# Kernel optimization log

Hardware: AMD Instinct MI355X
Metric: run time of the kernel (lower is better)

The kernel has to match this reference:

```python
import jax, jax.numpy as jnp
import numpy as np

E = 32          # n_routed_experts / num_local_experts
H = 1024        # hidden_size
I = 512         # moe_intermediate_size
G = 8           # n_group
TKG = 4         # topk_group
TOPK = 8        # num_experts_per_tok
NSH = 2         # n_shared_experts
SCALE = 2.5     # routed_scaling_factor


def setup_inputs() -> dict:
    key = jax.random.key(0)
    ks = jax.random.split(key, 10)
    s = 0.02
    return {
        "hidden_states": jax.random.normal(ks[0], (2, 1024, H), jnp.float32),
        # router: linear weight [E, H] and e_score_correction_bias [E]
        "gate_w": jax.random.normal(ks[1], (E, H), jnp.float32) * s,
        "gate_bias": jax.random.normal(ks[2], (E,), jnp.float32) * s,
        # routed experts (stacked SwiGLU weights, torch Linear layout [out, in])
        "w_gate": jax.random.normal(ks[3], (E, I, H), jnp.float32) * s,
        "w_up": jax.random.normal(ks[4], (E, I, H), jnp.float32) * s,
        "w_down": jax.random.normal(ks[5], (E, H, I), jnp.float32) * s,
        # shared experts: one MLP with intermediate = I * NSH
        "sh_gate": jax.random.normal(ks[6], (I * NSH, H), jnp.float32) * s,
        "sh_up": jax.random.normal(ks[7], (I * NSH, H), jnp.float32) * s,
        "sh_down": jax.random.normal(ks[8], (H, I * NSH), jnp.float32) * s,
    }


def reference(hidden_states, gate_w, gate_bias, w_gate, w_up, w_down,
              sh_gate, sh_up, sh_down):
    B, S, Hd = hidden_states.shape
    h = hidden_states.reshape(-1, Hd)                      # [T, H]

    # ---- router (DeepseekV3TopkRouter + route_tokens_to_experts) ----
    logits = h.astype(jnp.float32) @ gate_w.T              # [T, E]
    scores = jax.nn.sigmoid(logits)
    sc = scores + gate_bias                                # scores_for_choice
    # group score = sum of top-2 expert scores within each group
    grp = sc.reshape(-1, G, E // G)                        # [T, G, E/G]
    group_scores = jax.lax.top_k(grp, 2)[0].sum(-1)        # [T, G]
    gidx = jax.lax.top_k(group_scores, TKG)[1]             # [T, TKG]
    gmask = jnp.sum(jax.nn.one_hot(gidx, G, dtype=sc.dtype), axis=1)  # [T, G]
    smask = jnp.repeat(gmask, E // G, axis=1)              # [T, E]
    masked = jnp.where(smask > 0, sc, jnp.zeros_like(sc))  # masked_fill(~mask, 0)
    tki = jax.lax.top_k(masked, TOPK)[1]                   # [T, TOPK]
    tkw = jnp.take_along_axis(scores, tki, axis=1)         # gather raw sigmoid scores
    tkw = tkw / (tkw.sum(-1, keepdims=True) + 1e-20)       # norm_topk_prob
    tkw = tkw * SCALE

    # ---- dispatch-compute-combine (experts_forward) ----
    # combine[t, e] = sum_k tkw[t, k] * [tki[t, k] == e]
    combine = (jax.nn.one_hot(tki, E, dtype=tkw.dtype) * tkw[..., None]).sum(1)  # [T, E]
    g = jax.nn.silu(jnp.einsum('th,eih->tei', h, w_gate))  # [T, E, I]
    u = jnp.einsum('th,eih->tei', h, w_up)                 # [T, E, I]
    routed = jnp.einsum('tei,ehi->th', g * u * combine[:, :, None], w_down)  # [T, H]

    # ---- shared experts ----
    sg = jax.nn.silu(h @ sh_gate.T)
    shared = (sg * (h @ sh_up.T)) @ sh_down.T              # [T, H]

    return (routed + shared).reshape(B, S, Hd)
```

## Files before the change

kernel.cpp:

```cpp
#include <hip/hip_runtime.h>
#include <hip/hip_bf16.h>
#include <cstdint>

#define E_ 32
#define H_ 1024
#define I_ 512
#define G_ 8
#define NSH_ 2
#define SCALE_ 2.5f
#define NROUTED (E_ * I_)
#define PADCAP (16384 + E_ * 128)

typedef unsigned short u16;
using bf16x8_t = __attribute__((ext_vector_type(8))) __bf16;
using f32x4_t  = __attribute__((ext_vector_type(4))) float;

__device__ __forceinline__ u16 f2bf(float x) {
  union { float f; uint32_t u; } v; v.f = x;
  uint32_t u = v.u;
  uint32_t r = (u + 0x7fffu + ((u >> 16) & 1u)) >> 16;
  return (u16)r;
}
__device__ __forceinline__ float bf2f(u16 x) {
  union { uint32_t u; float f; } v; v.u = ((uint32_t)x) << 16; return v.f;
}

__device__ __forceinline__ void load_lds16(const void* g, void* l) {
  __builtin_amdgcn_global_load_lds(
      (const __attribute__((address_space(1))) unsigned int*)g,
      (__attribute__((address_space(3))) unsigned int*)l,
      16, 0, 0);
}

#define OFF_BU   16777216L
#define OFF_BD   33554432L
#define OFF_BSHG 50331648L
#define OFF_BSHU 51380224L
#define OFF_BSHD 52428800L
#define WBF_TOT  53477376L

#define W4_WG  4194304L
#define W4_WU  8388608L
#define W4_WD  12582912L
#define W4_SHG 12845056L
#define W4_SHU 13107200L
#define W4_TOT 13369344L
__global__ void prep_kernel(const float* __restrict__ gw, float* __restrict__ gwT,
                            int* __restrict__ counts, int* __restrict__ cursor,
                            int* __restrict__ qheads,
                            int* __restrict__ tok_list, float* __restrict__ wt_list,
                            const float* __restrict__ wg, const float* __restrict__ wu,
                            const float* __restrict__ wd, const float* __restrict__ shg,
                            const float* __restrict__ shu, const float* __restrict__ shd,
                            u16* __restrict__ wbf) {
  long i0 = (long)blockIdx.x * blockDim.x + threadIdx.x;
  if (i0 < H_ * E_) {
    int k = (int)(i0 >> 5), e = (int)(i0 & 31);
    gwT[i0] = gw[(long)e * H_ + k];
  }
  if (i0 < PADCAP) { tok_list[i0] = 0; wt_list[i0] = 0.f; }
  if (i0 < E_) { counts[i0] = 0; cursor[i0] = 0; }
  if (i0 < 2) qheads[i0] = 0;

  long stride = (long)gridDim.x * blockDim.x;
  for (long i = i0; i < W4_TOT; i += stride) {
    const float* s; long off; long dofs;
    if (i < W4_WG)       { s = wg;  off = i;            dofs = off * 4; }
    else if (i < W4_WU)  { s = wu;  off = i - W4_WG;    dofs = OFF_BU + off * 4; }
    else if (i < W4_WD)  { s = wd;  off = i - W4_WU;    dofs = OFF_BD + off * 4; }
    else if (i < W4_SHG) { s = shg; off = i - W4_WD;    dofs = OFF_BSHG + off * 4; }
    else if (i < W4_SHU) { s = shu; off = i - W4_SHG;   dofs = OFF_BSHU + off * 4; }
    else                 { s = shd; off = i - W4_SHU;   dofs = OFF_BSHD + off * 4; }
    float4 v = ((const float4*)s)[off];
    ushort4 o;
    o.x = f2bf(v.x); o.y = f2bf(v.y); o.z = f2bf(v.z); o.w = f2bf(v.w);
    *(ushort4*)(wbf + dofs) = o;
  }
}

__global__ __launch_bounds__(256) void logits_kernel(
    const float* __restrict__ h, const float* __restrict__ gwT,
    float* __restrict__ lpart,
    u16* __restrict__ hbf, int T) {
  __shared__ float shh[64][128];
  __shared__ float shw[128][E_];
  const int tid = threadIdx.x;
  const int t0 = blockIdx.x * 64;
  const int k0 = blockIdx.y * 128;
  #pragma unroll
  for (int i = 0; i < 8; ++i) {
    int c = tid + 256 * i;
    int row = c >> 5, col = c & 31;
    float4 v = *(const float4*)(h + (size_t)(t0 + row) * H_ + k0 + col * 4);
    *(float4*)(&shh[row][col * 4]) = v;
    ushort4 o;
    o.x = f2bf(v.x); o.y = f2bf(v.y); o.z = f2bf(v.z); o.w = f2bf(v.w);
    *(ushort4*)(hbf + (size_t)(t0 + row) * H_ + k0 + col * 4) = o;
  }
  #pragma unroll
  for (int i = 0; i < 4; ++i) {
    int c = tid + 256 * i;
    int row = c >> 3, col = c & 7;
    *(float4*)(&shw[row][col * 4]) =
        *(const float4*)(gwT + (size_t)(k0 + row) * E_ + col * 4);
  }
  __syncthreads();
  const int e = tid & 31;
  const int tb = (tid >> 5) * 8;
  float acc[8] = {0.f, 0.f, 0.f, 0.f, 0.f, 0.f, 0.f, 0.f};
  #pragma unroll 4
  for (int k = 0; k < 128; ++k) {
    float wv = shw[k][e];
    #pragma unroll
    for (int j = 0; j < 8; ++j) acc[j] += shh[tb + j][k] * wv;
  }
  #pragma unroll
  for (int j = 0; j < 8; ++j)
    lpart[((size_t)blockIdx.y * T + (t0 + tb + j)) * E_ + e] = acc[j];
}

__global__ __launch_bounds__(256) void topk_kernel(
    const float* __restrict__ lpart, const float* __restrict__ gb,
    int* __restrict__ idx8, float* __restrict__ wt8, int* __restrict__ counts,
    int T) {
  const int tid = threadIdx.x;
  const int l = tid & 63, wid = tid >> 6;
  const int e = l & 31, half = l >> 5;
  const int t = blockIdx.x * 8 + wid * 2 + half;

  float lg = 0.f;
  #pragma unroll
  for (int s = 0; s < 8; ++s) lg += lpart[((size_t)s * T + t) * E_ + e];
  float score = 1.f / (1.f + __expf(-lg));
  float sc = score + gb[e];

  float x1 = __shfl_xor(sc, 1);
  float x2 = __shfl_xor(sc, 2);
  float x3 = __shfl_xor(sc, 3);
  float hi1 = fmaxf(sc, x1), lo1 = fminf(sc, x1);
  float hi2 = fmaxf(x2, x3), lo2 = fminf(x2, x3);
  float m1 = fmaxf(hi1, hi2);
  float m2 = (hi1 >= hi2) ? fmaxf(lo1, hi2) : fmaxf(lo2, hi1);
  float gs = m1 + m2;

  float ga[8];
  #pragma unroll
  for (int g = 0; g < 8; ++g) ga[g] = __shfl(gs, (half << 5) + g * 4);
  unsigned gm = 0;
  #pragma unroll
  for (int r = 0; r < 4; ++r) {
    float bv = -1e30f; int bi = 0;
    #pragma unroll
    for (int g = 0; g < 8; ++g)
      if (!((gm >> g) & 1u) && ga[g] > bv) { bv = ga[g]; bi = g; }
    gm |= 1u << bi;
  }
  float msk = ((gm >> (e >> 2)) & 1u) ? sc : 0.f;

  float wsum = 0.f, myw = 0.f;
  int myi = 0;
  #pragma unroll
  for (int r = 0; r < 8; ++r) {
    float av = msk; int ai = e;
    #pragma unroll
    for (int m = 16; m; m >>= 1) {
      float ov = __shfl_xor(av, m);
      int oi = __shfl_xor(ai, m);
      if (ov > av || (ov == av && oi < ai)) { av = ov; ai = oi; }
    }
    float wscore = __shfl(score, (half << 5) + ai);
    wsum += wscore;
    if (e == r) { myi = ai; myw = wscore; }
    if (e == ai) msk = 0.f;
  }
  float inv = SCALE_ / (wsum + 1e-20f);
  if (e < 8) {
    idx8[(size_t)t * 8 + e] = myi;
    wt8[(size_t)t * 8 + e] = myw * inv;
    atomicAdd(&counts[myi], 1);
  }
}

__global__ void fill_kernel(const int* __restrict__ idx8, const float* __restrict__ wt8,
                            const int* __restrict__ counts, int* __restrict__ cursor,
                            int* __restrict__ tok_list, float* __restrict__ wt_list,
                            int* __restrict__ pair_pos, int npair) {
  int i = blockIdx.x * blockDim.x + threadIdx.x;
  if (i >= npair) return;
  int e = idx8[i];
  int offz = 0;
  for (int k = 0; k < E_; ++k) {
    if (k == e) break;
    offz += ((counts[k] + 127) >> 7) << 7;
  }
  int p = atomicAdd(&cursor[e], 1);
  int slot = offz + p;
  tok_list[slot] = i >> 3;
  wt_list[slot] = wt8[i];
  pair_pos[i] = slot;
}

__global__ __launch_bounds__(256, 2) void p1_kernel(
    const u16* __restrict__ hbf,
    const u16* __restrict__ wbf,
    const int* __restrict__ counts,
    const int* __restrict__ tok_list, const float* __restrict__ wt_list,
    int* __restrict__ qheads,
    u16* __restrict__ gu,
    u16* __restrict__ gu_sh,
    int T) {
  __shared__ u16 lsA[2][128 * 32];
  __shared__ u16 lsB0[2][128 * 32];
  __shared__ u16 lsB1[2][128 * 32];
  __shared__ int s_tok[128];
  __shared__ float s_wt[128];
  __shared__ int s_off[E_], s_ntt[E_];
  __shared__ int s_tot, s_tile;

  const int tid = threadIdx.x;
  if (tid == 0) {
    int run = 0, tot = 0;
    for (int e = 0; e < E_; ++e) {
      s_off[e] = run;
      int nt = (counts[e] + 127) >> 7;
      s_ntt[e] = nt;
      run += nt << 7;
      tot += nt * 4;
    }
    s_tot = tot + (T / 128) * 8;
  }

  const int w = tid >> 6, l = tid & 63;
  const int wr = w >> 1, wc = w & 1;
  const int lr = l & 15, lh = l >> 4;
  const int rdblk = (lh ^ ((lr >> 1) & 3)) << 3;

  const int c0 = tid, c1 = tid + 256;
  const int row0 = c0 >> 2, cb0 = c0 & 3, scb0 = cb0 ^ ((row0 >> 1) & 3);
  const int row1 = c1 >> 2, cb1 = c1 & 3, scb1 = cb1 ^ ((row1 >> 1) & 3);

  for (;;) {
    __syncthreads();
    if (tid == 0) s_tile = atomicAdd(&qheads[0], 1);
    __syncthreads();
    int q = s_tile;
    if (q >= s_tot) break;

    int z = 0, rem = q;
    for (; z < E_; ++z) { int t = s_ntt[z] * 4; if (rem < t) break; rem -= t; }
    const bool sh_e = (z == E_);
    int tt, nb;
    if (sh_e) { tt = rem >> 3; nb = rem & 7; }
    else      { tt = rem >> 2; nb = rem & 3; }
    const int off = sh_e ? 0 : s_off[z];

    if (tid < 128) {
      if (sh_e) { s_tok[tid] = tt * 128 + tid; s_wt[tid] = 1.0f; }
      else {
        int slot = off + tt * 128 + tid;
        s_tok[tid] = tok_list[slot];
        s_wt[tid] = wt_list[slot];
      }
    }
    __syncthreads();

    const u16* Bg = sh_e ? (wbf + OFF_BSHG + (size_t)(nb * 128) * H_)
                         : (wbf + ((size_t)z * I_ + nb * 128) * H_);
    const u16* Bu = sh_e ? (wbf + OFF_BSHU + (size_t)(nb * 128) * H_)
                         : (wbf + OFF_BU + ((size_t)z * I_ + nb * 128) * H_);
    const u16* A0 = hbf + (size_t)s_tok[row0] * H_ + scb0 * 8;
    const u16* A1 = hbf + (size_t)s_tok[row1] * H_ + scb1 * 8;

    f32x4_t acc0[4][4], acc1[4][4];
    #pragma unroll
    for (int m = 0; m < 4; ++m)
      #pragma unroll
      for (int n = 0; n < 4; ++n) {
        acc0[m][n] = (f32x4_t){0.f, 0.f, 0.f, 0.f};
        acc1[m][n] = (f32x4_t){0.f, 0.f, 0.f, 0.f};
      }

    auto stage = [&](int b, int k0) {
      load_lds16(A0 + k0, (char*)&lsA[b][0] + c0 * 16);
      load_lds16(A1 + k0, (char*)&lsA[b][0] + c1 * 16);
      load_lds16(Bg + (size_t)row0 * H_ + k0 + scb0 * 8, (char*)&lsB0[b][0] + c0 * 16);
      load_lds16(Bg + (size_t)row1 * H_ + k0 + scb1 * 8, (char*)&lsB0[b][0] + c1 * 16);
      load_lds16(Bu + (size_t)row0 * H_ + k0 + scb0 * 8, (char*)&lsB1[b][0] + c0 * 16);
      load_lds16(Bu + (size_t)row1 * H_ + k0 + scb1 * 8, (char*)&lsB1[b][0] + c1 * 16);
    };
    auto compute = [&](int b) {
      bf16x8_t af[4], b0f[4], b1f[4];
      #pragma unroll
      for (int m = 0; m < 4; ++m)
        af[m] = *(const bf16x8_t*)(&lsA[b][0] + (wr * 64 + m * 16 + lr) * 32 + rdblk);
      #pragma unroll
      for (int n = 0; n < 4; ++n) {
        b0f[n] = *(const bf16x8_t*)(&lsB0[b][0] + (wc * 64 + n * 16 + lr) * 32 + rdblk);
        b1f[n] = *(const bf16x8_t*)(&lsB1[b][0] + (wc * 64 + n * 16 + lr) * 32 + rdblk);
      }
      #pragma unroll
      for (int m = 0; m < 4; ++m)
        #pragma unroll
        for (int n = 0; n < 4; ++n) {
          acc0[m][n] = __builtin_amdgcn_mfma_f32_16x16x32_bf16(af[m], b0f[n], acc0[m][n], 0, 0, 0);
          acc1[m][n] = __builtin_amdgcn_mfma_f32_16x16x32_bf16(af[m], b1f[n], acc1[m][n], 0, 0, 0);
        }
    };

    stage(0, 0);
    __syncthreads();
    int cur = 0;
    #pragma unroll 1
    for (int s = 0; s < 32; ++s) {
      if (s < 31) stage(cur ^ 1, (s + 1) * 32);
      compute(cur);
      __syncthreads();
      cur ^= 1;
    }

    const int ldo = sh_e ? (I_ * NSH_) : I_;
    u16* outp = sh_e ? (gu_sh + (size_t)(tt * 128) * ldo + nb * 128)
                     : (gu + (size_t)(off + tt * 128) * ldo + nb * 128);
    #pragma unroll
    for (int m = 0; m < 4; ++m) {
      #pragma unroll
      for (int n = 0; n < 4; ++n) {
        int col = wc * 64 + n * 16 + lr;
        #pragma unroll
        for (int j = 0; j < 4; ++j) {
          int trow = wr * 64 + m * 16 + lh * 4 + j;
          float gv = acc0[m][n][j], uv = acc1[m][n][j];
          float sv = gv / (1.f + __expf(-gv));
          outp[(size_t)trow * ldo + col] = f2bf(sv * uv * s_wt[trow]);
        }
      }
    }
  }
}

__global__ __launch_bounds__(256, 3) void p2_kernel(
    const u16* __restrict__ gu, const u16* __restrict__ gu_sh,
    const u16* __restrict__ wbf,
    const int* __restrict__ counts,
    int* __restrict__ qheads,
    u16* __restrict__ part,
    u16* __restrict__ part_sh,
    int T) {
  __shared__ u16 lsA[2][128 * 32];
  __shared__ u16 lsB[2][128 * 32];
  __shared__ int s_off[E_], s_ntt[E_];
  __shared__ int s_tot, s_tile;

  const int tid = threadIdx.x;
  if (tid == 0) {
    int run = 0, tot = 0;
    for (int e = 0; e < E_; ++e) {
      s_off[e] = run;
      int nt = (counts[e] + 127) >> 7;
      s_ntt[e] = nt;
      run += nt << 7;
      tot += nt * 8;
    }
    s_tot = tot + (T / 128) * 8;
  }

  const int w = tid >> 6, l = tid & 63;
  const int wr = w >> 1, wc = w & 1;
  const int lr = l & 15, lh = l >> 4;
  const int rdblk = (lh ^ ((lr >> 1) & 3)) << 3;

  const int c0 = tid, c1 = tid + 256;
  const int row0 = c0 >> 2, cb0 = c0 & 3, scb0 = cb0 ^ ((row0 >> 1) & 3);
  const int row1 = c1 >> 2, cb1 = c1 & 3, scb1 = cb1 ^ ((row1 >> 1) & 3);

  for (;;) {
    __syncthreads();
    if (tid == 0) s_tile = atomicAdd(&qheads[1], 1);
    __syncthreads();
    int q = s_tile;
    if (q >= s_tot) break;

    int z = 0, rem = q;
    for (; z < E_; ++z) { int t = s_ntt[z] * 8; if (rem < t) break; rem -= t; }
    const bool sh_e = (z == E_);
    int tt = rem >> 3, nb = rem & 7;

    const int K = sh_e ? (I_ * NSH_) : I_;
    const int NT = K / 32;
    const u16* Ab = sh_e ? (gu_sh + (size_t)(tt * 128) * K)
                         : (gu + (size_t)(s_off[z] + tt * 128) * K);
    const u16* Bb = sh_e ? (wbf + OFF_BSHD + (size_t)(nb * 128) * K)
                         : (wbf + OFF_BD + (size_t)z * H_ * I_ + (size_t)(nb * 128) * K);
    u16* outp = sh_e ? (part_sh + (size_t)(tt * 128) * H_ + nb * 128)
                     : (part + (size_t)(s_off[z] + tt * 128) * H_ + nb * 128);

    f32x4_t acc[4][4];
    #pragma unroll
    for (int m = 0; m < 4; ++m)
      #pragma unroll
      for (int n = 0; n < 4; ++n) acc[m][n] = (f32x4_t){0.f, 0.f, 0.f, 0.f};

    auto stage = [&](int b, int k0) {
      load_lds16(Ab + (size_t)row0 * K + k0 + scb0 * 8, (char*)&lsA[b][0] + c0 * 16);
      load_lds16(Ab + (size_t)row1 * K + k0 + scb1 * 8, (char*)&lsA[b][0] + c1 * 16);
      load_lds16(Bb + (size_t)row0 * K + k0 + scb0 * 8, (char*)&lsB[b][0] + c0 * 16);
      load_lds16(Bb + (size_t)row1 * K + k0 + scb1 * 8, (char*)&lsB[b][0] + c1 * 16);
    };
    auto compute = [&](int b) {
      bf16x8_t af[4], bf[4];
      #pragma unroll
      for (int m = 0; m < 4; ++m)
        af[m] = *(const bf16x8_t*)(&lsA[b][0] + (wr * 64 + m * 16 + lr) * 32 + rdblk);
      #pragma unroll
      for (int n = 0; n < 4; ++n)
        bf[n] = *(const bf16x8_t*)(&lsB[b][0] + (wc * 64 + n * 16 + lr) * 32 + rdblk);
      #pragma unroll
      for (int m = 0; m < 4; ++m)
        #pragma unroll
        for (int n = 0; n < 4; ++n)
          acc[m][n] = __builtin_amdgcn_mfma_f32_16x16x32_bf16(af[m], bf[n], acc[m][n], 0, 0, 0);
    };

    stage(0, 0);
    __syncthreads();
    int cur = 0;
    #pragma unroll 1
    for (int s = 0; s < NT; ++s) {
      if (s < NT - 1) stage(cur ^ 1, (s + 1) * 32);
      compute(cur);
      __syncthreads();
      cur ^= 1;
    }

    #pragma unroll
    for (int m = 0; m < 4; ++m) {
      #pragma unroll
      for (int n = 0; n < 4; ++n) {
        int col = wc * 64 + n * 16 + lr;
        #pragma unroll
        for (int j = 0; j < 4; ++j) {
          int trow = wr * 64 + m * 16 + lh * 4 + j;
          outp[(size_t)trow * H_ + col] = f2bf(acc[m][n][j]);
        }
      }
    }
  }
}

__global__ void combine_kernel(const u16* __restrict__ part, const u16* __restrict__ part_sh,
                               const int* __restrict__ pair_pos, float* __restrict__ out) {
  int t = blockIdx.x;
  int h = threadIdx.x * 4;
  int pp[8];
  #pragma unroll
  for (int s = 0; s < 8; ++s) pp[s] = pair_pos[(long)t * 8 + s];
  ushort4 v = *(const ushort4*)(part_sh + (size_t)t * H_ + h);
  float a0 = bf2f(v.x), a1 = bf2f(v.y), a2 = bf2f(v.z), a3 = bf2f(v.w);
  #pragma unroll
  for (int s = 0; s < 8; ++s) {
    ushort4 u = *(const ushort4*)(part + (size_t)pp[s] * H_ + h);
    a0 += bf2f(u.x); a1 += bf2f(u.y); a2 += bf2f(u.z); a3 += bf2f(u.w);
  }
  float4 o = {a0, a1, a2, a3};
  *(float4*)(out + (size_t)t * H_ + h) = o;
}

extern "C" void kernel_launch(void* const* d_in, const int* in_sizes, int n_in,
                              void* d_out, int out_size, void* d_ws, size_t ws_size,
                              hipStream_t stream) {
  const float* hs  = (const float*)d_in[0];
  const float* gw  = (const float*)d_in[1];
  const float* gb  = (const float*)d_in[2];
  const float* wg  = (const float*)d_in[3];
  const float* wu  = (const float*)d_in[4];
  const float* wd  = (const float*)d_in[5];
  const float* shg = (const float*)d_in[6];
  const float* shu = (const float*)d_in[7];
  const float* shd = (const float*)d_in[8];
  float* out = (float*)d_out;

  const int T = in_sizes[0] / H_;

  char* ws = (char*)d_ws;
  size_t off = 0;
  auto alloc = [&](size_t bytes) {
    char* p = ws + off;
    off += (bytes + 255) & ~(size_t)255;
    return p;
  };
  int*   counts   = (int*)alloc(E_ * 4);
  int*   cursor   = (int*)alloc(E_ * 4);
  int*   qheads   = (int*)alloc(2 * 4);
  int*   idx8     = (int*)alloc((size_t)T * 8 * 4);
  float* wt8      = (float*)alloc((size_t)T * 8 * 4);
  int*   pair_pos = (int*)alloc((size_t)T * 8 * 4);
  int*   tok_list = (int*)alloc(PADCAP * 4);
  float* wt_list  = (float*)alloc(PADCAP * 4);
  float* gwT      = (float*)alloc((size_t)H_ * E_ * 4);
  float* lpart    = (float*)alloc((size_t)8 * T * E_ * 4);
  u16* hbf     = (u16*)alloc((size_t)T * H_ * 2);
  u16* wbf     = (u16*)alloc((size_t)WBF_TOT * 2);
  u16* gu      = (u16*)alloc((size_t)PADCAP * I_ * 2);
  u16* gu_sh   = (u16*)alloc((size_t)T * I_ * NSH_ * 2);
  u16* part    = (u16*)alloc((size_t)PADCAP * H_ * 2);
  u16* part_sh = (u16*)alloc((size_t)T * H_ * 2);
  if (off > ws_size) return;

  hipLaunchKernelGGL(prep_kernel, dim3(4096), dim3(256), 0, stream,
                     gw, gwT, counts, cursor, qheads, tok_list, wt_list,
                     wg, wu, wd, shg, shu, shd, wbf);

  hipLaunchKernelGGL(logits_kernel, dim3(T / 64, 8), dim3(256), 0, stream,
                     hs, gwT, lpart, hbf, T);

  hipLaunchKernelGGL(topk_kernel, dim3(T / 8), dim3(256), 0, stream,
                     lpart, gb, idx8, wt8, counts, T);

  hipLaunchKernelGGL(fill_kernel, dim3((T * 8 + 255) / 256), dim3(256), 0, stream,
                     idx8, wt8, counts, cursor, tok_list, wt_list, pair_pos, T * 8);

  hipLaunchKernelGGL(p1_kernel, dim3(512), dim3(256), 0, stream,
                     hbf, wbf, counts, tok_list, wt_list, qheads, gu, gu_sh, T);

  hipLaunchKernelGGL(p2_kernel, dim3(768), dim3(256), 0, stream,
                     gu, gu_sh, wbf, counts, qheads, part, part_sh, T);

  hipLaunchKernelGGL(combine_kernel, dim3(T), dim3(256), 0, stream,
                     part, part_sh, pair_pos, out);
}
```

Baseline: 268.5 us.

## Triple-buffer LDS staging in both expert GEMM kernels with one barrier per step

Both grouped GEMM kernels move from double to triple LDS buffering. The fetch runs two K-steps ahead, and explicit vmcnt waits plus a single s_barrier per iteration replace the old trailing __syncthreads. The goal is to hide more global-load latency and remove one full sync per K-step. The cost is more LDS per block, which could cut occupancy, and the hand-counted vmcnt values must match the number of loads issued per stage.

```diff
diff --git a/kernel.cpp b/kernel.cpp
--- a/kernel.cpp
+++ b/kernel.cpp
@@ -209,9 +209,9 @@
     u16* __restrict__ gu,
     u16* __restrict__ gu_sh,
     int T) {
-  __shared__ u16 lsA[2][128 * 32];
-  __shared__ u16 lsB0[2][128 * 32];
-  __shared__ u16 lsB1[2][128 * 32];
+  __shared__ u16 lsA[3][128 * 32];
+  __shared__ u16 lsB0[3][128 * 32];
+  __shared__ u16 lsB1[3][128 * 32];
   __shared__ int s_tok[128];
   __shared__ float s_wt[128];
   __shared__ int s_off[E_], s_ntt[E_];
@@ -280,7 +280,8 @@
         acc1[m][n] = (f32x4_t){0.f, 0.f, 0.f, 0.f};
       }
 
-    auto stage = [&](int b, int k0) {
+    auto stage = [&](int b, int ks) {
+      int k0 = ks * 32;
       load_lds16(A0 + k0, (char*)&lsA[b][0] + c0 * 16);
       load_lds16(A1 + k0, (char*)&lsA[b][0] + c1 * 16);
       load_lds16(Bg + (size_t)row0 * H_ + k0 + scb0 * 8, (char*)&lsB0[b][0] + c0 * 16);
@@ -308,15 +309,19 @@
     };
 
     stage(0, 0);
-    __syncthreads();
-    int cur = 0;
+    stage(1, 1);
+    int b0 = 0, b1 = 1, b2 = 2;
     #pragma unroll 1
-    for (int s = 0; s < 32; ++s) {
-      if (s < 31) stage(cur ^ 1, (s + 1) * 32);
-      compute(cur);
-      __syncthreads();
-      cur ^= 1;
-    }
+    for (int s = 0; s < 31; ++s) {
+      asm volatile("s_waitcnt vmcnt(6)" ::: "memory");
+      __builtin_amdgcn_s_barrier();
+      compute(b0);
+      if (s < 30) stage(b2, s + 2);
+      int tb = b0; b0 = b1; b1 = b2; b2 = tb;
+    }
+    asm volatile("s_waitcnt vmcnt(0)" ::: "memory");
+    __builtin_amdgcn_s_barrier();
+    compute(b0);
 
     const int ldo = sh_e ? (I_ * NSH_) : I_;
     u16* outp = sh_e ? (gu_sh + (size_t)(tt * 128) * ldo + nb * 128)
@@ -346,8 +351,8 @@
     u16* __restrict__ part,
     u16* __restrict__ part_sh,
     int T) {
-  __shared__ u16 lsA[2][128 * 32];
-  __shared__ u16 lsB[2][128 * 32];
+  __shared__ u16 lsA[3][128 * 32];
+  __shared__ u16 lsB[3][128 * 32];
   __shared__ int s_off[E_], s_ntt[E_];
   __shared__ int s_tot, s_tile;
 
@@ -400,7 +405,8 @@
       #pragma unroll
       for (int n = 0; n < 4; ++n) acc[m][n] = (f32x4_t){0.f, 0.f, 0.f, 0.f};
 
-    auto stage = [&](int b, int k0) {
+    auto stage = [&](int b, int ks) {
+      int k0 = ks * 32;
       load_lds16(Ab + (size_t)row0 * K + k0 + scb0 * 8, (char*)&lsA[b][0] + c0 * 16);
       load_lds16(Ab + (size_t)row1 * K + k0 + scb1 * 8, (char*)&lsA[b][0] + c1 * 16);
       load_lds16(Bb + (size_t)row0 * K + k0 + scb0 * 8, (char*)&lsB[b][0] + c0 * 16);
@@ -422,15 +428,19 @@
     };
 
     stage(0, 0);
-    __syncthreads();
-    int cur = 0;
+    stage(1, 1);
+    int b0 = 0, b1 = 1, b2 = 2;
     #pragma unroll 1
-    for (int s = 0; s < NT; ++s) {
-      if (s < NT - 1) stage(cur ^ 1, (s + 1) * 32);
-      compute(cur);
-      __syncthreads();
-      cur ^= 1;
-    }
+    for (int s = 0; s < NT - 1; ++s) {
+      asm volatile("s_waitcnt vmcnt(4)" ::: "memory");
+      __builtin_amdgcn_s_barrier();
+      compute(b0);
+      if (s + 2 < NT) stage(b2, s + 2);
+      int tb = b0; b0 = b1; b1 = b2; b2 = tb;
+    }
+    asm volatile("s_waitcnt vmcnt(0)" ::: "memory");
+    __builtin_amdgcn_s_barrier();
+    compute(b0);
 
     #pragma unroll
     for (int m = 0; m < 4; ++m) {
```

Measured after the change: 266.4 us. About the same (-0.8%).

## Retile expert GEMMs to BK=64 single-buffered with N-major tile order

Applied to the files above, without the earlier changes.

Both grouped GEMM kernels move from a double-buffered K=32 pipeline to a single-buffered K=64 stage with an 8-way XOR swizzle. p1 narrows its N tile from 128 to 64 so it fits three blocks per CU. Tile indices are reordered so consecutive tiles share the same weight slice across token tiles, which should improve L2 reuse of expert weights. Persistent grid sizes grow to match the higher occupancy. Dropping the double buffer loses the overlap of loads with compute inside a block, and the design relies on the extra resident blocks to hide that latency instead.

```diff
diff --git a/kernel.cpp b/kernel.cpp
--- a/kernel.cpp
+++ b/kernel.cpp
@@ -200,7 +200,7 @@
   pair_pos[i] = slot;
 }
 
-__global__ __launch_bounds__(256, 2) void p1_kernel(
+__global__ __launch_bounds__(256, 3) void p1_kernel(
     const u16* __restrict__ hbf,
     const u16* __restrict__ wbf,
     const int* __restrict__ counts,
@@ -209,145 +209,11 @@
     u16* __restrict__ gu,
     u16* __restrict__ gu_sh,
     int T) {
-  __shared__ u16 lsA[2][128 * 32];
-  __shared__ u16 lsB0[2][128 * 32];
-  __shared__ u16 lsB1[2][128 * 32];
+  __shared__ u16 lsA[128 * 64];
+  __shared__ u16 lsB0[64 * 64];
+  __shared__ u16 lsB1[64 * 64];
   __shared__ int s_tok[128];
   __shared__ float s_wt[128];
-  __shared__ int s_off[E_], s_ntt[E_];
-  __shared__ int s_tot, s_tile;
-
-  const int tid = threadIdx.x;
-  if (tid == 0) {
-    int run = 0, tot = 0;
-    for (int e = 0; e < E_; ++e) {
-      s_off[e] = run;
-      int nt = (counts[e] + 127) >> 7;
-      s_ntt[e] = nt;
-      run += nt << 7;
-      tot += nt * 4;
-    }
-    s_tot = tot + (T / 128) * 8;
-  }
-
-  const int w = tid >> 6, l = tid & 63;
-  const int wr = w >> 1, wc = w & 1;
-  const int lr = l & 15, lh = l >> 4;
-  const int rdblk = (lh ^ ((lr >> 1) & 3)) << 3;
-
-  const int c0 = tid, c1 = tid + 256;
-  const int row0 = c0 >> 2, cb0 = c0 & 3, scb0 = cb0 ^ ((row0 >> 1) & 3);
-  const int row1 = c1 >> 2, cb1 = c1 & 3, scb1 = cb1 ^ ((row1 >> 1) & 3);
-
-  for (;;) {
-    __syncthreads();
-    if (tid == 0) s_tile = atomicAdd(&qheads[0], 1);
-    __syncthreads();
-    int q = s_tile;
-    if (q >= s_tot) break;
-
-    int z = 0, rem = q;
-    for (; z < E_; ++z) { int t = s_ntt[z] * 4; if (rem < t) break; rem -= t; }
-    const bool sh_e = (z == E_);
-    int tt, nb;
-    if (sh_e) { tt = rem >> 3; nb = rem & 7; }
-    else      { tt = rem >> 2; nb = rem & 3; }
-    const int off = sh_e ? 0 : s_off[z];
-
-    if (tid < 128) {
-      if (sh_e) { s_tok[tid] = tt * 128 + tid; s_wt[tid] = 1.0f; }
-      else {
-        int slot = off + tt * 128 + tid;
-        s_tok[tid] = tok_list[slot];
-        s_wt[tid] = wt_list[slot];
-      }
-    }
-    __syncthreads();
-
-    const u16* Bg = sh_e ? (wbf + OFF_BSHG + (size_t)(nb * 128) * H_)
-                         : (wbf + ((size_t)z * I_ + nb * 128) * H_);
-    const u16* Bu = sh_e ? (wbf + OFF_BSHU + (size_t)(nb * 128) * H_)
-                         : (wbf + OFF_BU + ((size_t)z * I_ + nb * 128) * H_);
-    const u16* A0 = hbf + (size_t)s_tok[row0] * H_ + scb0 * 8;
-    const u16* A1 = hbf + (size_t)s_tok[row1] * H_ + scb1 * 8;
-
-    f32x4_t acc0[4][4], acc1[4][4];
-    #pragma unroll
-    for (int m = 0; m < 4; ++m)
-      #pragma unroll
-      for (int n = 0; n < 4; ++n) {
-        acc0[m][n] = (f32x4_t){0.f, 0.f, 0.f, 0.f};
-        acc1[m][n] = (f32x4_t){0.f, 0.f, 0.f, 0.f};
-      }
-
-    auto stage = [&](int b, int k0) {
-      load_lds16(A0 + k0, (char*)&lsA[b][0] + c0 * 16);
-      load_lds16(A1 + k0, (char*)&lsA[b][0] + c1 * 16);
-      load_lds16(Bg + (size_t)row0 * H_ + k0 + scb0 * 8, (char*)&lsB0[b][0] + c0 * 16);
-      load_lds16(Bg + (size_t)row1 * H_ + k0 + scb1 * 8, (char*)&lsB0[b][0] + c1 * 16);
-      load_lds16(Bu + (size_t)row0 * H_ + k0 + scb0 * 8, (char*)&lsB1[b][0] + c0 * 16);
-      load_lds16(Bu + (size_t)row1 * H_ + k0 + scb1 * 8, (char*)&lsB1[b][0] + c1 * 16);
-    };
-    auto compute = [&](int b) {
-      bf16x8_t af[4], b0f[4], b1f[4];
-      #pragma unroll
-      for (int m = 0; m < 4; ++m)
-        af[m] = *(const bf16x8_t*)(&lsA[b][0] + (wr * 64 + m * 16 + lr) * 32 + rdblk);
-      #pragma unroll
-      for (int n = 0; n < 4; ++n) {
-        b0f[n] = *(const bf16x8_t*)(&lsB0[b][0] + (wc * 64 + n * 16 + lr) * 32 + rdblk);
-        b1f[n] = *(const bf16x8_t*)(&lsB1[b][0] + (wc * 64 + n * 16 + lr) * 32 + rdblk);
-      }
-      #pragma unroll
-      for (int m = 0; m < 4; ++m)
-        #pragma unroll
-        for (int n = 0; n < 4; ++n) {
-          acc0[m][n] = __builtin_amdgcn_mfma_f32_16x16x32_bf16(af[m], b0f[n], acc0[m][n], 0, 0, 0);
-          acc1[m][n] = __builtin_amdgcn_mfma_f32_16x16x32_bf16(af[m], b1f[n], acc1[m][n], 0, 0, 0);
-        }
-    };
-
-    stage(0, 0);
-    __syncthreads();
-    int cur = 0;
-    #pragma unroll 1
-    for (int s = 0; s < 32; ++s) {
-      if (s < 31) stage(cur ^ 1, (s + 1) * 32);
-      compute(cur);
-      __syncthreads();
-      cur ^= 1;
-    }
-
-    const int ldo = sh_e ? (I_ * NSH_) : I_;
-    u16* outp = sh_e ? (gu_sh + (size_t)(tt * 128) * ldo + nb * 128)
-                     : (gu + (size_t)(off + tt * 128) * ldo + nb * 128);
-    #pragma unroll
-    for (int m = 0; m < 4; ++m) {
-      #pragma unroll
-      for (int n = 0; n < 4; ++n) {
-        int col = wc * 64 + n * 16 + lr;
-        #pragma unroll
-        for (int j = 0; j < 4; ++j) {
-          int trow = wr * 64 + m * 16 + lh * 4 + j;
-          float gv = acc0[m][n][j], uv = acc1[m][n][j];
-          float sv = gv / (1.f + __expf(-gv));
-          outp[(size_t)trow * ldo + col] = f2bf(sv * uv * s_wt[trow]);
-        }
-      }
-    }
-  }
-}
-
-__global__ __launch_bounds__(256, 3) void p2_kernel(
-    const u16* __restrict__ gu, const u16* __restrict__ gu_sh,
-    const u16* __restrict__ wbf,
-    const int* __restrict__ counts,
-    int* __restrict__ qheads,
-    u16* __restrict__ part,
-    u16* __restrict__ part_sh,
-    int T) {
-  __shared__ u16 lsA[2][128 * 32];
-  __shared__ u16 lsB[2][128 * 32];
   __shared__ int s_off[E_], s_ntt[E_];
   __shared__ int s_tot, s_tile;
 
@@ -361,17 +227,144 @@
       run += nt << 7;
       tot += nt * 8;
     }
-    s_tot = tot + (T / 128) * 8;
+    s_tot = tot + (T / 128) * 16;
   }
 
   const int w = tid >> 6, l = tid & 63;
   const int wr = w >> 1, wc = w & 1;
   const int lr = l & 15, lh = l >> 4;
-  const int rdblk = (lh ^ ((lr >> 1) & 3)) << 3;
-
-  const int c0 = tid, c1 = tid + 256;
-  const int row0 = c0 >> 2, cb0 = c0 & 3, scb0 = cb0 ^ ((row0 >> 1) & 3);
-  const int row1 = c1 >> 2, cb1 = c1 & 3, scb1 = cb1 ^ ((row1 >> 1) & 3);
+  const int sw = lr & 7;
+
+  for (;;) {
+    __syncthreads();
+    if (tid == 0) s_tile = atomicAdd(&qheads[0], 1);
+    __syncthreads();
+    int q = s_tile;
+    if (q >= s_tot) break;
+
+    int z = 0, rem = q;
+    for (; z < E_; ++z) { int t = s_ntt[z] * 8; if (rem < t) break; rem -= t; }
+    const bool sh_e = (z == E_);
+    int tt, nb;
+    if (sh_e) { nb = rem >> 4; tt = rem & 15; }
+    else      { int nt = s_ntt[z]; nb = rem / nt; tt = rem - nb * nt; }
+    const int off = sh_e ? 0 : s_off[z];
+
+    if (tid < 128) {
+      if (sh_e) { s_tok[tid] = tt * 128 + tid; s_wt[tid] = 1.0f; }
+      else {
+        int slot = off + tt * 128 + tid;
+        s_tok[tid] = tok_list[slot];
+        s_wt[tid] = wt_list[slot];
+      }
+    }
+    __syncthreads();
+
+    const u16* Bg = sh_e ? (wbf + OFF_BSHG + (size_t)(nb * 64) * H_)
+                         : (wbf + ((size_t)z * I_ + nb * 64) * H_);
+    const u16* Bu = sh_e ? (wbf + OFF_BSHU + (size_t)(nb * 64) * H_)
+                         : (wbf + OFF_BU + ((size_t)z * I_ + nb * 64) * H_);
+
+    f32x4_t acc0[4][2], acc1[4][2];
+    #pragma unroll
+    for (int m = 0; m < 4; ++m)
+      #pragma unroll
+      for (int n = 0; n < 2; ++n) {
+        acc0[m][n] = (f32x4_t){0.f, 0.f, 0.f, 0.f};
+        acc1[m][n] = (f32x4_t){0.f, 0.f, 0.f, 0.f};
+      }
+
+    for (int k0 = 0; k0 < H_; k0 += 64) {
+      #pragma unroll
+      for (int i = 0; i < 4; ++i) {
+        int c = tid + 256 * i;
+        int row = c >> 3, cb = c & 7;
+        int scb = cb ^ (row & 7);
+        load_lds16(hbf + (size_t)s_tok[row] * H_ + k0 + scb * 8, (char*)lsA + c * 16);
+      }
+      #pragma unroll
+      for (int i = 0; i < 2; ++i) {
+        int c = tid + 256 * i;
+        int row = c >> 3, cb = c & 7;
+        int scb = cb ^ (row & 7);
+        load_lds16(Bg + (size_t)row * H_ + k0 + scb * 8, (char*)lsB0 + c * 16);
+        load_lds16(Bu + (size_t)row * H_ + k0 + scb * 8, (char*)lsB1 + c * 16);
+      }
+      __syncthreads();
+      #pragma unroll
+      for (int kk = 0; kk < 64; kk += 32) {
+        const int sb = kk >> 3;
+        const int blk = ((sb + lh) ^ sw) << 3;
+        bf16x8_t af[4], b0f[2], b1f[2];
+        #pragma unroll
+        for (int m = 0; m < 4; ++m)
+          af[m] = *(const bf16x8_t*)(lsA + (wr * 64 + m * 16 + lr) * 64 + blk);
+        #pragma unroll
+        for (int n = 0; n < 2; ++n) {
+          b0f[n] = *(const bf16x8_t*)(lsB0 + (wc * 32 + n * 16 + lr) * 64 + blk);
+          b1f[n] = *(const bf16x8_t*)(lsB1 + (wc * 32 + n * 16 + lr) * 64 + blk);
+        }
+        #pragma unroll
+        for (int m = 0; m < 4; ++m)
+          #pragma unroll
+          for (int n = 0; n < 2; ++n) {
+            acc0[m][n] = __builtin_amdgcn_mfma_f32_16x16x32_bf16(af[m], b0f[n], acc0[m][n], 0, 0, 0);
+            acc1[m][n] = __builtin_amdgcn_mfma_f32_16x16x32_bf16(af[m], b1f[n], acc1[m][n], 0, 0, 0);
+          }
+      }
+      __syncthreads();
+    }
+
+    const int ldo = sh_e ? (I_ * NSH_) : I_;
+    u16* outp = sh_e ? (gu_sh + (size_t)(tt * 128) * ldo + nb * 64)
+                     : (gu + (size_t)(off + tt * 128) * ldo + nb * 64);
+    #pragma unroll
+    for (int m = 0; m < 4; ++m) {
+      #pragma unroll
+      for (int n = 0; n < 2; ++n) {
+        int col = wc * 32 + n * 16 + lr;
+        #pragma unroll
+        for (int j = 0; j < 4; ++j) {
+          int trow = wr * 64 + m * 16 + lh * 4 + j;
+          float gv = acc0[m][n][j], uv = acc1[m][n][j];
+          float sv = gv / (1.f + __expf(-gv));
+          outp[(size_t)trow * ldo + col] = f2bf(sv * uv * s_wt[trow]);
+        }
+      }
+    }
+  }
+}
+
+__global__ __launch_bounds__(256, 3) void p2_kernel(
+    const u16* __restrict__ gu, const u16* __restrict__ gu_sh,
+    const u16* __restrict__ wbf,
+    const int* __restrict__ counts,
+    int* __restrict__ qheads,
+    u16* __restrict__ part,
+    u16* __restrict__ part_sh,
+    int T) {
+  __shared__ u16 lsA[128 * 64];
+  __shared__ u16 lsB[128 * 64];
+  __shared__ int s_off[E_], s_ntt[E_];
+  __shared__ int s_tot, s_tile;
+
+  const int tid = threadIdx.x;
+  if (tid == 0) {
+    int run = 0, tot = 0;
+    for (int e = 0; e < E_; ++e) {
+      s_off[e] = run;
+      int nt = (counts[e] + 127) >> 7;
+      s_ntt[e] = nt;
+      run += nt << 7;
+      tot += nt * 8;
+    }
+    s_tot = tot + (T / 128) * 8;
+  }
+
+  const int w = tid >> 6, l = tid & 63;
+  const int wr = w >> 1, wc = w & 1;
+  const int lr = l & 15, lh = l >> 4;
+  const int sw = lr & 7;
 
   for (;;) {
     __syncthreads();
@@ -383,10 +376,12 @@
     int z = 0, rem = q;
     for (; z < E_; ++z) { int t = s_ntt[z] * 8; if (rem < t) break; rem -= t; }
     const bool sh_e = (z == E_);
-    int tt = rem >> 3, nb = rem & 7;
+    int tt, nb;
+    if (sh_e) { nb = rem >> 4; tt = rem & 15; }
+    else      { int nt = s_ntt[z]; nb = rem / nt; tt = rem - nb * nt; }
 
     const int K = sh_e ? (I_ * NSH_) : I_;
-    const int NT = K / 32;
+    const int NT = K / 64;
     const u16* Ab = sh_e ? (gu_sh + (size_t)(tt * 128) * K)
                          : (gu + (size_t)(s_off[z] + tt * 128) * K);
     const u16* Bb = sh_e ? (wbf + OFF_BSHD + (size_t)(nb * 128) * K)
@@ -400,36 +395,35 @@
       #pragma unroll
       for (int n = 0; n < 4; ++n) acc[m][n] = (f32x4_t){0.f, 0.f, 0.f, 0.f};
 
-    auto stage = [&](int b, int k0) {
-      load_lds16(Ab + (size_t)row0 * K + k0 + scb0 * 8, (char*)&lsA[b][0] + c0 * 16);
-      load_lds16(Ab + (size_t)row1 * K + k0 + scb1 * 8, (char*)&lsA[b][0] + c1 * 16);
-      load_lds16(Bb + (size_t)row0 * K + k0 + scb0 * 8, (char*)&lsB[b][0] + c0 * 16);
-      load_lds16(Bb + (size_t)row1 * K + k0 + scb1 * 8, (char*)&lsB[b][0] + c1 * 16);
-    };
-    auto compute = [&](int b) {
-      bf16x8_t af[4], bf[4];
-      #pragma unroll
-      for (int m = 0; m < 4; ++m)
-        af[m] = *(const bf16x8_t*)(&lsA[b][0] + (wr * 64 + m * 16 + lr) * 32 + rdblk);
-      #pragma unroll
-      for (int n = 0; n < 4; ++n)
-        bf[n] = *(const bf16x8_t*)(&lsB[b][0] + (wc * 64 + n * 16 + lr) * 32 + rdblk);
-      #pragma unroll
-      for (int m = 0; m < 4; ++m)
+    for (int s = 0; s < NT; ++s) {
+      int k0 = s * 64;
+      #pragma unroll
+      for (int i = 0; i < 4; ++i) {
+        int c = tid + 256 * i;
+        int row = c >> 3, cb = c & 7;
+        int scb = cb ^ (row & 7);
+        load_lds16(Ab + (size_t)row * K + k0 + scb * 8, (char*)lsA + c * 16);
+        load_lds16(Bb + (size_t)row * K + k0 + scb * 8, (char*)lsB + c * 16);
+      }
+      __syncthreads();
+      #pragma unroll
+      for (int kk = 0; kk < 64; kk += 32) {
+        const int sb = kk >> 3;
+        const int blk = ((sb + lh) ^ sw) << 3;
+        bf16x8_t af[4], bf[4];
+        #pragma unroll
+        for (int m = 0; m < 4; ++m)
+          af[m] = *(const bf16x8_t*)(lsA + (wr * 64 + m * 16 + lr) * 64 + blk);
         #pragma unroll
         for (int n = 0; n < 4; ++n)
-          acc[m][n] = __builtin_amdgcn_mfma_f32_16x16x32_bf16(af[m], bf[n], acc[m][n], 0, 0, 0);
-    };
-
-    stage(0, 0);
-    __syncthreads();
-    int cur = 0;
-    #pragma unroll 1
-    for (int s = 0; s < NT; ++s) {
-      if (s < NT - 1) stage(cur ^ 1, (s + 1) * 32);
-      compute(cur);
+          bf[n] = *(const bf16x8_t*)(lsB + (wc * 64 + n * 16 + lr) * 64 + blk);
+        #pragma unroll
+        for (int m = 0; m < 4; ++m)
+          #pragma unroll
+          for (int n = 0; n < 4; ++n)
+            acc[m][n] = __builtin_amdgcn_mfma_f32_16x16x32_bf16(af[m], bf[n], acc[m][n], 0, 0, 0);
+      }
       __syncthreads();
-      cur ^= 1;
     }
 
     #pragma unroll
@@ -519,10 +513,10 @@
   hipLaunchKernelGGL(fill_kernel, dim3((T * 8 + 255) / 256), dim3(256), 0, stream,
                      idx8, wt8, counts, cursor, tok_list, wt_list, pair_pos, T * 8);
 
-  hipLaunchKernelGGL(p1_kernel, dim3(512), dim3(256), 0, stream,
+  hipLaunchKernelGGL(p1_kernel, dim3(1280), dim3(256), 0, stream,
                      hbf, wbf, counts, tok_list, wt_list, qheads, gu, gu_sh, T);
 
-  hipLaunchKernelGGL(p2_kernel, dim3(768), dim3(256), 0, stream,
+  hipLaunchKernelGGL(p2_kernel, dim3(1152), dim3(256), 0, stream,
                      gu, gu_sh, wbf, counts, qheads, part, part_sh, T);
 
   hipLaunchKernelGGL(combine_kernel, dim3(T), dim3(256), 0, stream,
```

Result: slower. 291.8 us (+8.7%).
